# Performance work log

Measured on AMD Instinct MI355X. Metric: run time of the kernel, lower is better.

The kernel has to match this reference:

```python
import jax, jax.numpy as jnp
import numpy as np

B, H, W, C = 64, 56, 56, 192
NH, WS, SS = 6, 7, 3          # heads, window size, shift size
N = WS * WS                   # tokens per window = 49
NW = (H // WS) * (W // WS)    # windows per image = 64
HD = C // NH                  # head dim = 32
SCALE = HD ** -0.5
EPS = 1e-5


def _rel_pos_index():
    coords = np.stack(np.meshgrid(np.arange(WS), np.arange(WS), indexing='ij'))  # [2,WS,WS]
    flat = coords.reshape(2, -1)                                                  # [2,N]
    rel = (flat[:, :, None] - flat[:, None, :]).transpose(1, 2, 0)                # [N,N,2]
    rel[..., 0] += WS - 1
    rel[..., 1] += WS - 1
    rel[..., 0] *= 2 * WS - 1
    return jnp.asarray(rel.sum(-1))  # [N,N] int

REL_IDX = _rel_pos_index()


def _shift_mask():
    # standard Swin shifted-window attention mask: 0 within region, -100 across
    img = np.zeros((H, W), dtype=np.float32)
    cnt = 0
    for hs in (slice(0, -WS), slice(-WS, -SS), slice(-SS, None)):
        for ws in (slice(0, -WS), slice(-WS, -SS), slice(-SS, None)):
            img[hs, ws] = cnt
            cnt += 1
    win = img.reshape(H // WS, WS, W // WS, WS).transpose(0, 2, 1, 3).reshape(NW, N)
    diff = win[:, None, :] - win[:, :, None]
    return jnp.asarray(np.where(diff != 0, -100.0, 0.0).astype(np.float32))  # [NW,N,N]


def setup_inputs() -> dict:
    key = jax.random.key(0)
    ks = jax.random.split(key, 8)
    s = 0.02
    return {
        'x': jax.random.normal(ks[0], (B, H, W, C), jnp.float32),
        'mask_matrix': _shift_mask(),
        'norm1_g': jnp.ones((C,), jnp.float32),
        'norm1_b': jnp.zeros((C,), jnp.float32),
        'qkv_w': jax.random.normal(ks[1], (3 * C, C), jnp.float32) * s,
        'qkv_b': jnp.zeros((3 * C,), jnp.float32),
        'rpb_table': jax.random.normal(ks[2], ((2 * WS - 1) ** 2, NH), jnp.float32) * s,
        'proj_w': jax.random.normal(ks[3], (C, C), jnp.float32) * s,
        'proj_b': jnp.zeros((C,), jnp.float32),
        'norm2_g': jnp.ones((C,), jnp.float32),
        'norm2_b': jnp.zeros((C,), jnp.float32),
        'fc1_w': jax.random.normal(ks[4], (4 * C, C), jnp.float32) * s,
        'fc1_b': jnp.zeros((4 * C,), jnp.float32),
        'fc2_w': jax.random.normal(ks[5], (C, 4 * C), jnp.float32) * s,
        'fc2_b': jnp.zeros((C,), jnp.float32),
    }


def _ln(x, g, b):
    m = jnp.mean(x, axis=-1, keepdims=True)
    v = jnp.mean(jnp.square(x - m), axis=-1, keepdims=True)
    return (x - m) * jax.lax.rsqrt(v + EPS) * g + b


def _block(x, mask_matrix, norm1_g, norm1_b, qkv_w, qkv_b, rpb_table,
           proj_w, proj_b, norm2_g, norm2_b, fc1_w, fc1_b, fc2_w, fc2_b):
    shortcut = x
    xn = _ln(x, norm1_g, norm1_b)
    # cyclic shift
    xs = jnp.roll(xn, (-SS, -SS), axis=(1, 2))
    # window partition -> [B*NW, N, C]
    win = xs.reshape(B, H // WS, WS, W // WS, WS, C).transpose(0, 1, 3, 2, 4, 5).reshape(B * NW, N, C)
    # qkv projection
    qkv = jnp.einsum('wnc,dc->wnd', win, qkv_w) + qkv_b           # [B*NW, N, 3C]
    qkv = qkv.reshape(B * NW, N, 3, NH, HD).transpose(2, 0, 3, 1, 4)
    q, k, v = qkv[0], qkv[1], qkv[2]                               # [B*NW, NH, N, HD]
    attn = jnp.einsum('whqd,whkd->whqk', q * SCALE, k)             # [B*NW, NH, N, N]
    # relative position bias gather
    bias = rpb_table[REL_IDX.reshape(-1)].reshape(N, N, NH).transpose(2, 0, 1)  # [NH,N,N]
    attn = attn + bias[None]
    # shifted-window mask
    attn = attn.reshape(B, NW, NH, N, N) + mask_matrix[None, :, None]
    attn = jax.nn.softmax(attn.reshape(B * NW, NH, N, N), axis=-1)
    out = jnp.einsum('whqk,whkd->whqd', attn, v)                   # [B*NW, NH, N, HD]
    out = out.transpose(0, 2, 1, 3).reshape(B * NW, N, C)
    out = jnp.einsum('wnc,dc->wnd', out, proj_w) + proj_b
    # window reverse + reverse shift
    xr = out.reshape(B, H // WS, W // WS, WS, WS, C).transpose(0, 1, 3, 2, 4, 5).reshape(B, H, W, C)
    xr = jnp.roll(xr, (SS, SS), axis=(1, 2))
    x = shortcut + xr
    # MLP
    xn2 = _ln(x, norm2_g, norm2_b)
    h = jax.nn.gelu(jnp.einsum('bhwc,dc->bhwd', xn2, fc1_w) + fc1_b, approximate=False)
    x = x + jnp.einsum('bhwd,cd->bhwc', h, fc2_w) + fc2_b
    return x


def reference(x, mask_matrix, norm1_g, norm1_b, qkv_w, qkv_b, rpb_table,
              proj_w, proj_b, norm2_g, norm2_b, fc1_w, fc1_b, fc2_w, fc2_b):
    return _block(x, mask_matrix, norm1_g, norm1_b, qkv_w, qkv_b, rpb_table,
                  proj_w, proj_b, norm2_g, norm2_b, fc1_w, fc1_b, fc2_w, fc2_b)
```

## Files before the change

kernel.cpp:

```cpp
#include <hip/hip_runtime.h>
#include <hip/hip_bf16.h>
#include <math.h>

typedef __attribute__((ext_vector_type(8))) short s16x8;
typedef __attribute__((ext_vector_type(4))) float f32x4;

static constexpr float cSCALE = 0.17677669529663687f;

__device__ __forceinline__ float bf2f(unsigned short u) {
    union { unsigned int i; float f; } c; c.i = ((unsigned int)u) << 16; return c.f;
}
__device__ __forceinline__ unsigned short f2bf(float f) {
    union { float f; unsigned int i; } c; c.f = f;
    unsigned int r = c.i + (0x7fffu + ((c.i >> 16) & 1u));
    return (unsigned short)(r >> 16);
}
__device__ __forceinline__ unsigned pk2(float a, float b) {
    unsigned r;
    asm("v_cvt_pk_bf16_f32 %0, %1, %2" : "=v"(r) : "v"(a), "v"(b));
    return r;
}
__device__ __forceinline__ s16x8 cvt8(const float4 a, const float4 b) {
    s16x8 r;
    r[0]=(short)f2bf(a.x); r[1]=(short)f2bf(a.y); r[2]=(short)f2bf(a.z); r[3]=(short)f2bf(a.w);
    r[4]=(short)f2bf(b.x); r[5]=(short)f2bf(b.y); r[6]=(short)f2bf(b.z); r[7]=(short)f2bf(b.w);
    return r;
}
__device__ __forceinline__ float gelu_f(float t) {
    const float u = 1.5957691216057308f * t * (1.0f + 0.044715f * t * t);
    return t / (1.0f + __expf(-u));
}

#define GLDS16(gp, lp) __builtin_amdgcn_global_load_lds( \
    (const __attribute__((address_space(1))) void*)(gp), \
    (__attribute__((address_space(3))) void*)(lp), 16, 0, 0)

__device__ __forceinline__ void ln_frag(const float* __restrict__ rowp,
                                        const float* __restrict__ g,
                                        const float* __restrict__ b,
                                        int hi, s16x8* xa)
{
    float4 v[12];
    #pragma unroll
    for (int k = 0; k < 6; ++k) {
        v[2*k]   = *(const float4*)(rowp + k*32 + hi*8);
        v[2*k+1] = *(const float4*)(rowp + k*32 + hi*8 + 4);
    }
    float sm = 0.f, sq = 0.f;
    #pragma unroll
    for (int i = 0; i < 12; ++i) {
        sm += (v[i].x + v[i].y) + (v[i].z + v[i].w);
        sq += (v[i].x*v[i].x + v[i].y*v[i].y) + (v[i].z*v[i].z + v[i].w*v[i].w);
    }
    sm += __shfl_xor(sm, 16); sq += __shfl_xor(sq, 16);
    sm += __shfl_xor(sm, 32); sq += __shfl_xor(sq, 32);
    const float mean = sm * (1.0f/192.0f);
    const float rstd = rsqrtf(sq * (1.0f/192.0f) - mean*mean + 1e-5f);
    #pragma unroll
    for (int k = 0; k < 6; ++k) {
        const float4 ga = *(const float4*)(g + k*32 + hi*8);
        const float4 gb = *(const float4*)(g + k*32 + hi*8 + 4);
        const float4 ba = *(const float4*)(b + k*32 + hi*8);
        const float4 bb = *(const float4*)(b + k*32 + hi*8 + 4);
        union { s16x8 s; unsigned u[4]; } r;
        r.u[0] = pk2((v[2*k].x  -mean)*rstd*ga.x + ba.x, (v[2*k].y  -mean)*rstd*ga.y + ba.y);
        r.u[1] = pk2((v[2*k].z  -mean)*rstd*ga.z + ba.z, (v[2*k].w  -mean)*rstd*ga.w + ba.w);
        r.u[2] = pk2((v[2*k+1].x-mean)*rstd*gb.x + bb.x, (v[2*k+1].y-mean)*rstd*gb.y + bb.y);
        r.u[3] = pk2((v[2*k+1].z-mean)*rstd*gb.z + bb.z, (v[2*k+1].w-mean)*rstd*gb.w + bb.w);
        xa[k] = r.s;
    }
}

__global__ __launch_bounds__(256)
void pack_w(const float* __restrict__ qkvw, const float* __restrict__ pw,
            const float* __restrict__ f1w, const float* __restrict__ f2w,
            unsigned short* __restrict__ o)
{
    const int t = blockIdx.x * 256 + threadIdx.x;
    const int lane = t & 63, f = t >> 6;
    const int ln = lane & 15, ko = (lane >> 4) * 8;
    const float* src;
    if (f < 216) {
        const int h = f / 36, r = f - h * 36, nf = r / 6, kf = r - nf * 6;
        src = qkvw + (size_t)((nf >> 1) * 192 + h * 32 + (nf & 1) * 16 + ln) * 192 + kf * 32 + ko;
    } else if (f < 288) {
        const int g = f - 216, h = g / 12, nf = g - h * 12;
        src = pw + (size_t)(nf * 16 + ln) * 192 + h * 32 + ko;
    } else {
        const int g = f - 288;
        const int c = g / 24, r24 = g - c * 24;
        if (r24 < 12) {
            const int nf = r24 / 6, kf = r24 - nf * 6;
            src = f1w + (size_t)(c * 32 + nf * 16 + ln) * 192 + kf * 32 + ko;
        } else {
            const int nf = r24 - 12;
            src = f2w + (size_t)(nf * 16 + ln) * 768 + c * 32 + ko;
        }
    }
    *(s16x8*)(o + (size_t)t * 8) = cvt8(*(const float4*)src, *(const float4*)(src + 4));
}

__global__ __launch_bounds__(256)
void pack_bias(const float* __restrict__ mask, const float* __restrict__ rpb,
               unsigned short* __restrict__ o)
{
    const int wi = blockIdx.x / 6, h = blockIdx.x - wi * 6;
    for (int t = threadIdx.x; t < 49 * 64; t += 256) {
        const int n = t >> 6, mm = t & 63;
        const int ln = mm >> 2, nf = mm & 3;
        const int m = nf * 16 + ln;
        float v = -100.0f;
        if (m < 49) {
            const int p1 = n / 7, q1 = n - p1 * 7, p2 = m / 7, q2 = m - p2 * 7;
            const int ridx = (p1 - p2 + 6) * 13 + (q1 - q2 + 6);
            v = rpb[ridx * 6 + h] + mask[(size_t)wi * 2401 + n * 49 + m];
        }
        o[(size_t)(wi * 6 + h) * 3136 + t] = f2bf(v);
    }
}

__global__ __launch_bounds__(256, 4)
void swin_attn(const float* __restrict__ x, const float* __restrict__ g1,
               const float* __restrict__ b1, const unsigned short* __restrict__ wp,
               const unsigned short* __restrict__ bias_g,
               const float* __restrict__ qkvb, const float* __restrict__ pb,
               float* __restrict__ y)
{
    __shared__ __align__(16) unsigned short q_[64][40];
    __shared__ __align__(16) unsigned short o_[64][40];
    __shared__ __align__(16) unsigned short k2_[2][64][40];
    __shared__ __align__(16) unsigned short vt2_[2][32][72];
    __shared__ __align__(16) unsigned short p_[64][72];

    const s16x8* wv = (const s16x8*)wp;
    const int w  = blockIdx.x;
    const int bb = w >> 6, wi = w & 63;
    const int wh = wi >> 3, ww = wi & 7;
    const int tid = threadIdx.x, lane = tid & 63, wave = tid >> 6;
    const int ln = lane & 15, hi = lane >> 4, ko = hi * 8, ro = hi * 4;
    const int m0 = wave * 16;

    s16x8 xa[6];
    {
        const int t = m0 + ln;
        const int p = t / 7, q7 = t - p * 7;
        int i2 = wh * 7 + p + 3;  if (i2 >= 56) i2 -= 56;
        int j2 = ww * 7 + q7 + 3; if (j2 >= 56) j2 -= 56;
        const float* xr = x + ((size_t)(bb * 56 + i2) * 56 + j2) * 192;
        ln_frag(xr, g1, b1, hi, xa);
        if (t >= 49) {
            #pragma unroll
            for (int k = 0; k < 6; ++k) xa[k] = s16x8{0,0,0,0,0,0,0,0};
        }
    }

    auto qkv_head = [&](int hh) {
        const s16x8* wq = wv + ((size_t)(hh * 36) << 6);
        #pragma unroll
        for (int nf = 0; nf < 6; ++nf) {
            s16x8 bf6[6];
            #pragma unroll
            for (int kf = 0; kf < 6; ++kf) bf6[kf] = wq[(nf * 6 + kf) * 64 + lane];
            f32x4 a = f32x4{0.f,0.f,0.f,0.f};
            #pragma unroll
            for (int kf = 0; kf < 6; ++kf)
                a = __builtin_amdgcn_mfma_f32_16x16x32_bf16(xa[kf], bf6[kf], a, 0, 0, 0);
            const int col = nf * 16 + ln;
            if (nf < 2) {
                const float bq = qkvb[hh*32 + col];
                const unsigned lo = pk2((a[0]+bq)*cSCALE, (a[1]+bq)*cSCALE);
                const unsigned hh2 = pk2((a[2]+bq)*cSCALE, (a[3]+bq)*cSCALE);
                q_[m0+ro+0][col] = (unsigned short)lo;  q_[m0+ro+1][col] = (unsigned short)(lo >> 16);
                q_[m0+ro+2][col] = (unsigned short)hh2; q_[m0+ro+3][col] = (unsigned short)(hh2 >> 16);
            } else if (nf < 4) {
                const float bk = qkvb[192 + hh*32 + col - 32];
                const unsigned lo = pk2(a[0]+bk, a[1]+bk), hh2 = pk2(a[2]+bk, a[3]+bk);
                k2_[hh&1][m0+ro+0][col-32] = (unsigned short)lo;  k2_[hh&1][m0+ro+1][col-32] = (unsigned short)(lo >> 16);
                k2_[hh&1][m0+ro+2][col-32] = (unsigned short)hh2; k2_[hh&1][m0+ro+3][col-32] = (unsigned short)(hh2 >> 16);
            } else {
                const float bv = qkvb[384 + hh*32 + col - 64];
                const unsigned lo = pk2(a[0]+bv, a[1]+bv), hh2 = pk2(a[2]+bv, a[3]+bv);
                vt2_[hh&1][col-64][m0+ro+0] = (unsigned short)lo;  vt2_[hh&1][col-64][m0+ro+1] = (unsigned short)(lo >> 16);
                vt2_[hh&1][col-64][m0+ro+2] = (unsigned short)hh2; vt2_[hh&1][col-64][m0+ro+3] = (unsigned short)(hh2 >> 16);
            }
        }
    };

    qkv_head(0);

    f32x4 accp[12];
    #pragma unroll
    for (int i = 0; i < 12; ++i) accp[i] = f32x4{0.f,0.f,0.f,0.f};

    uint2 bb4[4];
    {
        const unsigned short* bg = bias_g + (size_t)(wi * 6) * 3136;
        #pragma unroll
        for (int i = 0; i < 4; ++i) {
            const int nc = min(m0 + ro + i, 48);
            bb4[i] = *(const uint2*)(bg + nc * 64 + ln * 4);
        }
    }

    for (int h = 0; h < 6; ++h) {
        __syncthreads();

        f32x4 s4[4];
        {
            const s16x8 aq = *(const s16x8*)&q_[m0 + ln][ko];
            #pragma unroll
            for (int nf = 0; nf < 4; ++nf) {
                const s16x8 bk = *(const s16x8*)&k2_[h & 1][nf * 16 + ln][ko];
                s4[nf] = __builtin_amdgcn_mfma_f32_16x16x32_bf16(aq, bk, f32x4{0.f,0.f,0.f,0.f}, 0, 0, 0);
            }
        }
        float inv4[4];
        #pragma unroll
        for (int i = 0; i < 4; ++i) {
            const int n = m0 + ro + i;
            const uint2 u = bb4[i];
            const float e0 = __expf(s4[0][i] + bf2f((unsigned short)(u.x)));
            const float e1 = __expf(s4[1][i] + bf2f((unsigned short)(u.x >> 16)));
            const float e2 = __expf(s4[2][i] + bf2f((unsigned short)(u.y)));
            const float e3 = __expf(s4[3][i] + bf2f((unsigned short)(u.y >> 16)));
            float ssum = (e0 + e1) + (e2 + e3);
            #pragma unroll
            for (int o = 1; o < 16; o <<= 1) ssum += __shfl_xor(ssum, o);
            inv4[i] = 1.0f / ssum;
            const unsigned plo = pk2(e0, e1), phi = pk2(e2, e3);
            p_[n][     ln] = (unsigned short)plo;
            p_[n][16 + ln] = (unsigned short)(plo >> 16);
            p_[n][32 + ln] = (unsigned short)phi;
            p_[n][48 + ln] = (unsigned short)(phi >> 16);
        }

        {
            const int hn = (h < 5) ? h + 1 : 5;
            const unsigned short* bg = bias_g + (size_t)(wi * 6 + hn) * 3136;
            #pragma unroll
            for (int i = 0; i < 4; ++i) {
                const int nc = min(m0 + ro + i, 48);
                bb4[i] = *(const uint2*)(bg + nc * 64 + ln * 4);
            }
        }

        f32x4 o2[2];
        o2[0] = f32x4{0.f,0.f,0.f,0.f}; o2[1] = f32x4{0.f,0.f,0.f,0.f};
        #pragma unroll
        for (int kf = 0; kf < 2; ++kf) {
            const s16x8 ap = *(const s16x8*)&p_[m0 + ln][kf * 32 + ko];
            #pragma unroll
            for (int nf = 0; nf < 2; ++nf) {
                const s16x8 bv = *(const s16x8*)&vt2_[h & 1][nf * 16 + ln][kf * 32 + ko];
                o2[nf] = __builtin_amdgcn_mfma_f32_16x16x32_bf16(ap, bv, o2[nf], 0, 0, 0);
            }
        }
        #pragma unroll
        for (int nf = 0; nf < 2; ++nf) {
            const int col = nf * 16 + ln;
            const unsigned lo = pk2(o2[nf][0] * inv4[0], o2[nf][1] * inv4[1]);
            const unsigned hh2 = pk2(o2[nf][2] * inv4[2], o2[nf][3] * inv4[3]);
            o_[m0+ro+0][col] = (unsigned short)lo;  o_[m0+ro+1][col] = (unsigned short)(lo >> 16);
            o_[m0+ro+2][col] = (unsigned short)hh2; o_[m0+ro+3][col] = (unsigned short)(hh2 >> 16);
        }

        if (h < 5) qkv_head(h + 1);

        {
            const s16x8 ao = *(const s16x8*)&o_[m0 + ln][ko];
            const s16x8* wpj = wv + ((size_t)(216 + h * 12) << 6);
            #pragma unroll
            for (int half = 0; half < 2; ++half) {
                s16x8 bf6[6];
                #pragma unroll
                for (int nf = 0; nf < 6; ++nf) bf6[nf] = wpj[(half * 6 + nf) * 64 + lane];
                #pragma unroll
                for (int nf = 0; nf < 6; ++nf)
                    accp[half * 6 + nf] = __builtin_amdgcn_mfma_f32_16x16x32_bf16(
                        ao, bf6[nf], accp[half * 6 + nf], 0, 0, 0);
            }
        }
    }

    #pragma unroll
    for (int i = 0; i < 4; ++i) {
        const int n = m0 + ro + i;
        if (n < 49) {
            const int p = n / 7, q7 = n - p * 7;
            int i2 = wh * 7 + p + 3;  if (i2 >= 56) i2 -= 56;
            int j2 = ww * 7 + q7 + 3; if (j2 >= 56) j2 -= 56;
            const size_t base = ((size_t)(bb * 56 + i2) * 56 + j2) * 192;
            #pragma unroll
            for (int nf = 0; nf < 12; ++nf) {
                const int col = nf * 16 + ln;
                y[base + col] = x[base + col] + pb[col] + accp[nf][i];
            }
        }
    }
}

__device__ __forceinline__ void stage24k(const unsigned short* __restrict__ wp, int c,
                                         unsigned short* dst, int tid) {
    const unsigned short* g = wp + (((size_t)(288 + c * 24)) << 9) + tid * 8;
    unsigned short* l = dst + tid * 8;
    #pragma unroll
    for (int i = 0; i < 3; ++i)
        GLDS16(g + i * 4096, l + i * 4096);
}

__global__ __launch_bounds__(512, 4)
void swin_mlp(const float* __restrict__ g2, const float* __restrict__ b2,
              const unsigned short* __restrict__ wp,
              const float* __restrict__ f1b, const float* __restrict__ f2b,
              float* __restrict__ y)
{
    __shared__ __align__(16) unsigned short wbuf[2][12288];
    __shared__ __align__(16) unsigned short hb[128][40];
    __shared__ float f1b_l[768];
    __shared__ float f2b_l[192];

    const int tid = threadIdx.x, lane = tid & 63, wave = tid >> 6;
    const int ln = lane & 15, hi = lane >> 4, ko = hi * 8, ro = hi * 4;
    const int m0 = wave * 16;
    const size_t r0 = (size_t)blockIdx.x * 128;

    for (int t = tid; t < 768; t += 512) f1b_l[t] = f1b[t];
    for (int t = tid; t < 192; t += 512) f2b_l[t] = f2b[t];

    s16x8 xa[6];
    ln_frag(y + (r0 + m0 + ln) * 192, g2, b2, hi, xa);

    stage24k(wp, 0, wbuf[0], tid);
    stage24k(wp, 1, wbuf[1], tid);
    asm volatile("s_waitcnt lgkmcnt(0)" ::: "memory");

    f32x4 acc2[12];
    #pragma unroll
    for (int i = 0; i < 12; ++i) acc2[i] = f32x4{0.f,0.f,0.f,0.f};

    for (int c = 0; c < 24; ++c) {
        if (c == 23) asm volatile("s_waitcnt vmcnt(0)" ::: "memory");
        else         asm volatile("s_waitcnt vmcnt(3)" ::: "memory");
        __builtin_amdgcn_s_barrier();

        const s16x8* wb = (const s16x8*)wbuf[c & 1];
        f32x4 acc1[2];
        acc1[0] = f32x4{0.f,0.f,0.f,0.f}; acc1[1] = f32x4{0.f,0.f,0.f,0.f};
        #pragma unroll
        for (int kf = 0; kf < 6; ++kf) {
            #pragma unroll
            for (int nf = 0; nf < 2; ++nf)
                acc1[nf] = __builtin_amdgcn_mfma_f32_16x16x32_bf16(
                    xa[kf], wb[(nf * 6 + kf) * 64 + lane], acc1[nf], 0, 0, 0);
        }
        #pragma unroll
        for (int nf = 0; nf < 2; ++nf) {
            const int col = nf * 16 + ln;
            const float bias = f1b_l[c * 32 + col];
            const unsigned lo = pk2(gelu_f(acc1[nf][0] + bias), gelu_f(acc1[nf][1] + bias));
            const unsigned hh2 = pk2(gelu_f(acc1[nf][2] + bias), gelu_f(acc1[nf][3] + bias));
            hb[m0+ro+0][col] = (unsigned short)lo;  hb[m0+ro+1][col] = (unsigned short)(lo >> 16);
            hb[m0+ro+2][col] = (unsigned short)hh2; hb[m0+ro+3][col] = (unsigned short)(hh2 >> 16);
        }
        const s16x8 ah = *(const s16x8*)&hb[m0 + ln][ko];
        #pragma unroll
        for (int nf = 0; nf < 12; ++nf)
            acc2[nf] = __builtin_amdgcn_mfma_f32_16x16x32_bf16(
                ah, wb[(12 + nf) * 64 + lane], acc2[nf], 0, 0, 0);

        if (c < 23) {
            __builtin_amdgcn_s_barrier();
            if (c < 22) stage24k(wp, c + 2, wbuf[c & 1], tid);
        }
    }

    #pragma unroll
    for (int i = 0; i < 4; ++i) {
        const int row = m0 + ro + i;
        float* yp = y + (r0 + row) * 192;
        #pragma unroll
        for (int nf = 0; nf < 12; ++nf) {
            const int col = nf * 16 + ln;
            yp[col] = yp[col] + f2b_l[col] + acc2[nf][i];
        }
    }
}

extern "C" void kernel_launch(void* const* d_in, const int* in_sizes, int n_in,
                              void* d_out, int out_size, void* d_ws, size_t ws_size,
                              hipStream_t stream) {
    (void)in_sizes; (void)n_in; (void)ws_size; (void)out_size;
    const float* x    = (const float*)d_in[0];
    const float* mask = (const float*)d_in[1];
    const float* g1   = (const float*)d_in[2];
    const float* b1   = (const float*)d_in[3];
    const float* qkvw = (const float*)d_in[4];
    const float* qkvb = (const float*)d_in[5];
    const float* rpb  = (const float*)d_in[6];
    const float* pw   = (const float*)d_in[7];
    const float* pb   = (const float*)d_in[8];
    const float* g2   = (const float*)d_in[9];
    const float* b2   = (const float*)d_in[10];
    const float* f1w  = (const float*)d_in[11];
    const float* f1b  = (const float*)d_in[12];
    const float* f2w  = (const float*)d_in[13];
    const float* f2b  = (const float*)d_in[14];
    float* y = (float*)d_out;
    unsigned short* wpk  = (unsigned short*)d_ws;
    unsigned short* bias = wpk + 442368;

    pack_w<<<dim3(216), dim3(256), 0, stream>>>(qkvw, pw, f1w, f2w, wpk);
    pack_bias<<<dim3(384), dim3(256), 0, stream>>>(mask, rpb, bias);
    swin_attn<<<dim3(64 * 64), dim3(256), 0, stream>>>(
        x, g1, b1, wpk, bias, qkvb, pb, y);
    swin_mlp<<<dim3(1568), dim3(512), 0, stream>>>(
        g2, b2, wpk, f1b, f2b, y);
}
```

Before: 530.7 us.

## Give each MLP wave two row tiles and merge the packing kernels

```diff
diff --git a/kernel.cpp b/kernel.cpp
--- a/kernel.cpp
+++ b/kernel.cpp
@@ -72,50 +72,49 @@
 }
 
 __global__ __launch_bounds__(256)
-void pack_w(const float* __restrict__ qkvw, const float* __restrict__ pw,
-            const float* __restrict__ f1w, const float* __restrict__ f2w,
-            unsigned short* __restrict__ o)
+void pack_all(const float* __restrict__ qkvw, const float* __restrict__ pw,
+              const float* __restrict__ f1w, const float* __restrict__ f2w,
+              const float* __restrict__ mask, const float* __restrict__ rpb,
+              unsigned short* __restrict__ o, unsigned short* __restrict__ ob)
 {
-    const int t = blockIdx.x * 256 + threadIdx.x;
-    const int lane = t & 63, f = t >> 6;
-    const int ln = lane & 15, ko = (lane >> 4) * 8;
-    const float* src;
-    if (f < 216) {
-        const int h = f / 36, r = f - h * 36, nf = r / 6, kf = r - nf * 6;
-        src = qkvw + (size_t)((nf >> 1) * 192 + h * 32 + (nf & 1) * 16 + ln) * 192 + kf * 32 + ko;
-    } else if (f < 288) {
-        const int g = f - 216, h = g / 12, nf = g - h * 12;
-        src = pw + (size_t)(nf * 16 + ln) * 192 + h * 32 + ko;
+    if (blockIdx.x < 216) {
+        const int t = blockIdx.x * 256 + threadIdx.x;
+        const int lane = t & 63, f = t >> 6;
+        const int ln = lane & 15, ko = (lane >> 4) * 8;
+        const float* src;
+        if (f < 216) {
+            const int h = f / 36, r = f - h * 36, nf = r / 6, kf = r - nf * 6;
+            src = qkvw + (size_t)((nf >> 1) * 192 + h * 32 + (nf & 1) * 16 + ln) * 192 + kf * 32 + ko;
+        } else if (f < 288) {
+            const int g = f - 216, h = g / 12, nf = g - h * 12;
+            src = pw + (size_t)(nf * 16 + ln) * 192 + h * 32 + ko;
+        } else {
+            const int g = f - 288;
+            const int c = g / 24, r24 = g - c * 24;
+            if (r24 < 12) {
+                const int nf = r24 / 6, kf = r24 - nf * 6;
+                src = f1w + (size_t)(c * 32 + nf * 16 + ln) * 192 + kf * 32 + ko;
+            } else {
+                const int nf = r24 - 12;
+                src = f2w + (size_t)(nf * 16 + ln) * 768 + c * 32 + ko;
+            }
+        }
+        *(s16x8*)(o + (size_t)t * 8) = cvt8(*(const float4*)src, *(const float4*)(src + 4));
     } else {
-        const int g = f - 288;
-        const int c = g / 24, r24 = g - c * 24;
-        if (r24 < 12) {
-            const int nf = r24 / 6, kf = r24 - nf * 6;
-            src = f1w + (size_t)(c * 32 + nf * 16 + ln) * 192 + kf * 32 + ko;
-        } else {
-            const int nf = r24 - 12;
-            src = f2w + (size_t)(nf * 16 + ln) * 768 + c * 32 + ko;
-        }
-    }
-    *(s16x8*)(o + (size_t)t * 8) = cvt8(*(const float4*)src, *(const float4*)(src + 4));
-}
-
-__global__ __launch_bounds__(256)
-void pack_bias(const float* __restrict__ mask, const float* __restrict__ rpb,
-               unsigned short* __restrict__ o)
-{
-    const int wi = blockIdx.x / 6, h = blockIdx.x - wi * 6;
-    for (int t = threadIdx.x; t < 49 * 64; t += 256) {
-        const int n = t >> 6, mm = t & 63;
-        const int ln = mm >> 2, nf = mm & 3;
-        const int m = nf * 16 + ln;
-        float v = -100.0f;
-        if (m < 49) {
-            const int p1 = n / 7, q1 = n - p1 * 7, p2 = m / 7, q2 = m - p2 * 7;
-            const int ridx = (p1 - p2 + 6) * 13 + (q1 - q2 + 6);
-            v = rpb[ridx * 6 + h] + mask[(size_t)wi * 2401 + n * 49 + m];
-        }
-        o[(size_t)(wi * 6 + h) * 3136 + t] = f2bf(v);
+        const int bid = blockIdx.x - 216;
+        const int wi = bid / 6, h = bid - wi * 6;
+        for (int t = threadIdx.x; t < 49 * 64; t += 256) {
+            const int n = t >> 6, mm = t & 63;
+            const int ln = mm >> 2, nf = mm & 3;
+            const int m = nf * 16 + ln;
+            float v = -100.0f;
+            if (m < 49) {
+                const int p1 = n / 7, q1 = n - p1 * 7, p2 = m / 7, q2 = m - p2 * 7;
+                const int ridx = (p1 - p2 + 6) * 13 + (q1 - q2 + 6);
+                v = rpb[ridx * 6 + h] + mask[(size_t)wi * 2401 + n * 49 + m];
+            }
+            ob[(size_t)(wi * 6 + h) * 3136 + t] = f2bf(v);
+        }
     }
 }
 
@@ -304,11 +303,11 @@
     const unsigned short* g = wp + (((size_t)(288 + c * 24)) << 9) + tid * 8;
     unsigned short* l = dst + tid * 8;
     #pragma unroll
-    for (int i = 0; i < 3; ++i)
-        GLDS16(g + i * 4096, l + i * 4096);
-}
-
-__global__ __launch_bounds__(512, 4)
+    for (int i = 0; i < 6; ++i)
+        GLDS16(g + i * 2048, l + i * 2048);
+}
+
+__global__ __launch_bounds__(256, 2)
 void swin_mlp(const float* __restrict__ g2, const float* __restrict__ b2,
               const unsigned short* __restrict__ wp,
               const float* __restrict__ f1b, const float* __restrict__ f2b,
@@ -321,52 +320,64 @@
 
     const int tid = threadIdx.x, lane = tid & 63, wave = tid >> 6;
     const int ln = lane & 15, hi = lane >> 4, ko = hi * 8, ro = hi * 4;
-    const int m0 = wave * 16;
+    const int m0 = wave * 32;
     const size_t r0 = (size_t)blockIdx.x * 128;
 
-    for (int t = tid; t < 768; t += 512) f1b_l[t] = f1b[t];
-    for (int t = tid; t < 192; t += 512) f2b_l[t] = f2b[t];
-
-    s16x8 xa[6];
-    ln_frag(y + (r0 + m0 + ln) * 192, g2, b2, hi, xa);
+    for (int t = tid; t < 768; t += 256) f1b_l[t] = f1b[t];
+    for (int t = tid; t < 192; t += 256) f2b_l[t] = f2b[t];
+
+    s16x8 xa[12];
+    ln_frag(y + (r0 + m0 +      ln) * 192, g2, b2, hi, xa);
+    ln_frag(y + (r0 + m0 + 16 + ln) * 192, g2, b2, hi, xa + 6);
 
     stage24k(wp, 0, wbuf[0], tid);
     stage24k(wp, 1, wbuf[1], tid);
     asm volatile("s_waitcnt lgkmcnt(0)" ::: "memory");
 
-    f32x4 acc2[12];
-    #pragma unroll
-    for (int i = 0; i < 12; ++i) acc2[i] = f32x4{0.f,0.f,0.f,0.f};
+    f32x4 acc2[24];
+    #pragma unroll
+    for (int i = 0; i < 24; ++i) acc2[i] = f32x4{0.f,0.f,0.f,0.f};
 
     for (int c = 0; c < 24; ++c) {
         if (c == 23) asm volatile("s_waitcnt vmcnt(0)" ::: "memory");
-        else         asm volatile("s_waitcnt vmcnt(3)" ::: "memory");
+        else         asm volatile("s_waitcnt vmcnt(6)" ::: "memory");
         __builtin_amdgcn_s_barrier();
 
         const s16x8* wb = (const s16x8*)wbuf[c & 1];
-        f32x4 acc1[2];
-        acc1[0] = f32x4{0.f,0.f,0.f,0.f}; acc1[1] = f32x4{0.f,0.f,0.f,0.f};
+        f32x4 acc1[4];
+        #pragma unroll
+        for (int i = 0; i < 4; ++i) acc1[i] = f32x4{0.f,0.f,0.f,0.f};
         #pragma unroll
         for (int kf = 0; kf < 6; ++kf) {
             #pragma unroll
-            for (int nf = 0; nf < 2; ++nf)
-                acc1[nf] = __builtin_amdgcn_mfma_f32_16x16x32_bf16(
-                    xa[kf], wb[(nf * 6 + kf) * 64 + lane], acc1[nf], 0, 0, 0);
+            for (int nf = 0; nf < 2; ++nf) {
+                const s16x8 b = wb[(nf * 6 + kf) * 64 + lane];
+                acc1[nf*2+0] = __builtin_amdgcn_mfma_f32_16x16x32_bf16(xa[kf],     b, acc1[nf*2+0], 0, 0, 0);
+                acc1[nf*2+1] = __builtin_amdgcn_mfma_f32_16x16x32_bf16(xa[6 + kf], b, acc1[nf*2+1], 0, 0, 0);
+            }
         }
         #pragma unroll
         for (int nf = 0; nf < 2; ++nf) {
             const int col = nf * 16 + ln;
             const float bias = f1b_l[c * 32 + col];
-            const unsigned lo = pk2(gelu_f(acc1[nf][0] + bias), gelu_f(acc1[nf][1] + bias));
-            const unsigned hh2 = pk2(gelu_f(acc1[nf][2] + bias), gelu_f(acc1[nf][3] + bias));
-            hb[m0+ro+0][col] = (unsigned short)lo;  hb[m0+ro+1][col] = (unsigned short)(lo >> 16);
-            hb[m0+ro+2][col] = (unsigned short)hh2; hb[m0+ro+3][col] = (unsigned short)(hh2 >> 16);
-        }
-        const s16x8 ah = *(const s16x8*)&hb[m0 + ln][ko];
-        #pragma unroll
-        for (int nf = 0; nf < 12; ++nf)
-            acc2[nf] = __builtin_amdgcn_mfma_f32_16x16x32_bf16(
-                ah, wb[(12 + nf) * 64 + lane], acc2[nf], 0, 0, 0);
+            #pragma unroll
+            for (int rs = 0; rs < 2; ++rs) {
+                const f32x4 a = acc1[nf*2+rs];
+                const int rb = m0 + rs * 16 + ro;
+                const unsigned lo = pk2(gelu_f(a[0] + bias), gelu_f(a[1] + bias));
+                const unsigned hh2 = pk2(gelu_f(a[2] + bias), gelu_f(a[3] + bias));
+                hb[rb+0][col] = (unsigned short)lo;  hb[rb+1][col] = (unsigned short)(lo >> 16);
+                hb[rb+2][col] = (unsigned short)hh2; hb[rb+3][col] = (unsigned short)(hh2 >> 16);
+            }
+        }
+        const s16x8 ah0 = *(const s16x8*)&hb[m0 +      ln][ko];
+        const s16x8 ah1 = *(const s16x8*)&hb[m0 + 16 + ln][ko];
+        #pragma unroll
+        for (int nf = 0; nf < 12; ++nf) {
+            const s16x8 b = wb[(12 + nf) * 64 + lane];
+            acc2[nf*2+0] = __builtin_amdgcn_mfma_f32_16x16x32_bf16(ah0, b, acc2[nf*2+0], 0, 0, 0);
+            acc2[nf*2+1] = __builtin_amdgcn_mfma_f32_16x16x32_bf16(ah1, b, acc2[nf*2+1], 0, 0, 0);
+        }
 
         if (c < 23) {
             __builtin_amdgcn_s_barrier();
@@ -375,13 +386,16 @@
     }
 
     #pragma unroll
-    for (int i = 0; i < 4; ++i) {
-        const int row = m0 + ro + i;
-        float* yp = y + (r0 + row) * 192;
-        #pragma unroll
-        for (int nf = 0; nf < 12; ++nf) {
-            const int col = nf * 16 + ln;
-            yp[col] = yp[col] + f2b_l[col] + acc2[nf][i];
+    for (int rs = 0; rs < 2; ++rs) {
+        #pragma unroll
+        for (int i = 0; i < 4; ++i) {
+            const int row = m0 + rs * 16 + ro + i;
+            float* yp = y + (r0 + row) * 192;
+            #pragma unroll
+            for (int nf = 0; nf < 12; ++nf) {
+                const int col = nf * 16 + ln;
+                yp[col] = yp[col] + f2b_l[col] + acc2[nf*2+rs][i];
+            }
         }
     }
 }
@@ -409,10 +423,9 @@
     unsigned short* wpk  = (unsigned short*)d_ws;
     unsigned short* bias = wpk + 442368;
 
-    pack_w<<<dim3(216), dim3(256), 0, stream>>>(qkvw, pw, f1w, f2w, wpk);
-    pack_bias<<<dim3(384), dim3(256), 0, stream>>>(mask, rpb, bias);
+    pack_all<<<dim3(600), dim3(256), 0, stream>>>(qkvw, pw, f1w, f2w, mask, rpb, wpk, bias);
     swin_attn<<<dim3(64 * 64), dim3(256), 0, stream>>>(
         x, g1, b1, wpk, bias, qkvb, pb, y);
-    swin_mlp<<<dim3(1568), dim3(512), 0, stream>>>(
+    swin_mlp<<<dim3(1568), dim3(256), 0, stream>>>(
         g2, b2, wpk, f1b, f2b, y);
 }
```

New measurement: 525.7 us. About the same (-0.9%).
